# Kernel tuning notes

Hardware: AMD Instinct MI355X
Metric: run time of the kernel (lower is better)

The kernel has to match this reference:

```python
import jax, jax.numpy as jnp
import numpy as np

M_BUCKETS = 2048  # input_features // q = 4096 // 2


def countsketch(x, hash_idx, rand_sgn, m=M_BUCKETS):
    # x: [N, D]; scatter-add signed columns into m buckets -> [N, m]
    return jnp.zeros((x.shape[0], m), x.dtype).at[:, hash_idx].add(x * rand_sgn[None, :])


def setup_inputs() -> dict:
    key = jax.random.key(0)
    k1, k2, k3, k4, k5 = jax.random.split(key, 5)
    B, D, O = 4096, 4096, 4096
    inp = jax.random.normal(k1, (B, D), dtype=jnp.float32)
    # match torch init: weight uniform(-sqrt(3)/sqrt(D), sqrt(3)/sqrt(D)), bias uniform(-1/sqrt(D), 1/sqrt(D))
    bound = 1.0 / np.sqrt(D)
    weight = jax.random.uniform(k2, (O, D), dtype=jnp.float32,
                                minval=-bound * np.sqrt(3.0), maxval=bound * np.sqrt(3.0))
    bias = jax.random.uniform(k3, (O,), dtype=jnp.float32, minval=-bound, maxval=bound)
    hash_idx = jax.random.randint(k4, (D,), 0, M_BUCKETS, dtype=jnp.int32)
    rand_sgn = (2.0 * jax.random.randint(k5, (D,), 0, 2).astype(jnp.float32) - 1.0)
    return {"input": inp, "weight": weight, "bias": bias,
            "hash_idx": hash_idx, "rand_sgn": rand_sgn}


def reference(input, weight, bias, hash_idx, rand_sgn):
    input_sketch = countsketch(input, hash_idx, rand_sgn)    # [B, m]
    weight_sketch = countsketch(weight, hash_idx, rand_sgn)  # [O, m]
    out = input_sketch @ weight_sketch.T + bias[None, :]     # [B, O]
    return out
```

## Files before the change

### kernel.cpp

```cpp
#include <hip/hip_runtime.h>
#include <hip/hip_bf16.h>
#include <stdint.h>

#define D_DIM     4096
#define MB        2048
#define NROWS     4096
#define K_DIM     MB

typedef __bf16 bf16x8 __attribute__((ext_vector_type(8)));
typedef float  floatx4 __attribute__((ext_vector_type(4)));

__device__ __forceinline__ void gld_lds16(const void* g, void* l) {
    __builtin_amdgcn_global_load_lds(
        (const __attribute__((address_space(1))) unsigned int*)g,
        (__attribute__((address_space(3))) unsigned int*)l,
        16, 0, 0);
}

__global__ __launch_bounds__(256) void build_csr(
    const int* __restrict__ hash_idx,
    int* __restrict__ csr_off,
    int* __restrict__ csr_col)
{
    __shared__ int cnt[MB];
    __shared__ int scan[MB];
    const int t = threadIdx.x;

    for (int k = t; k < MB; k += 256) cnt[k] = 0;
    __syncthreads();
    for (int j = t; j < D_DIM; j += 256) atomicAdd(&cnt[hash_idx[j]], 1);
    __syncthreads();
    for (int k = t; k < MB; k += 256) scan[k] = cnt[k];
    __syncthreads();
    for (int stride = 1; stride < MB; stride <<= 1) {
        int vals[8];
        #pragma unroll
        for (int i = 0; i < 8; ++i) {
            int k = t + 256 * i;
            vals[i] = (k >= stride) ? scan[k - stride] : 0;
        }
        __syncthreads();
        #pragma unroll
        for (int i = 0; i < 8; ++i) scan[t + 256 * i] += vals[i];
        __syncthreads();
    }
    for (int k = t; k < MB; k += 256) csr_off[k] = scan[k] - cnt[k];
    if (t == 0) csr_off[MB] = scan[MB - 1];
    for (int k = t; k < MB; k += 256) cnt[k] = scan[k] - cnt[k];
    __syncthreads();
    for (int j = t; j < D_DIM; j += 256) {
        int k = hash_idx[j];
        int pos = atomicAdd(&cnt[k], 1);
        csr_col[pos] = j;
    }
}

__global__ __launch_bounds__(256) void sketch_kernel(
    const float* __restrict__ input,
    const float* __restrict__ weight,
    const float* __restrict__ rand_sgn,
    const int* __restrict__ csr_off,
    const int* __restrict__ csr_col,
    __hip_bfloat16* __restrict__ sk_in,
    __hip_bfloat16* __restrict__ sk_w)
{
    __shared__ float row[D_DIM];
    const int b = blockIdx.x;
    const bool is_w = (b >= NROWS);
    const int r = is_w ? (b - NROWS) : b;
    const float* src = (is_w ? weight : input) + (size_t)r * D_DIM;
    __hip_bfloat16* dst = (is_w ? sk_w : sk_in) + (size_t)r * MB;
    const int t = threadIdx.x;

    const float4* src4 = (const float4*)src;
    const float4* sgn4 = (const float4*)rand_sgn;
    #pragma unroll
    for (int i = 0; i < 4; ++i) {
        int idx = t + 256 * i;
        float4 x = src4[idx], s = sgn4[idx];
        row[4 * idx + 0] = x.x * s.x;
        row[4 * idx + 1] = x.y * s.y;
        row[4 * idx + 2] = x.z * s.z;
        row[4 * idx + 3] = x.w * s.w;
    }
    __syncthreads();

    #pragma unroll
    for (int i = 0; i < 8; ++i) {
        int k = t + 256 * i;
        int o0 = csr_off[k], o1 = csr_off[k + 1];
        float sum = 0.f;
        for (int p = o0; p < o1; ++p) sum += row[csr_col[p]];
        dst[k] = __float2bfloat16(sum);
    }
}

__global__ __launch_bounds__(256) void gemm_bt_bias(
    const __hip_bfloat16* __restrict__ A,
    const __hip_bfloat16* __restrict__ B,
    const float* __restrict__ bias,
    float* __restrict__ C)
{
    __shared__ __align__(16) __hip_bfloat16 lA[128 * 32];
    __shared__ __align__(16) __hip_bfloat16 lB[128 * 32];

    const int t = threadIdx.x;
    const int lane = t & 63;
    const int wid  = t >> 6;
    const int warpM = wid & 1, warpN = wid >> 1;
    const int quad = lane >> 4;
    const int mrow = lane & 15;
    const int rowBase = blockIdx.y * 128;
    const int colBase = blockIdx.x * 128;

    const int sr = t >> 2;
    const int sc = (t & 3) << 3;
    const __hip_bfloat16* gA = A + (size_t)(rowBase + sr) * K_DIM + sc;
    const __hip_bfloat16* gB = B + (size_t)(colBase + sr) * K_DIM + sc;
    __hip_bfloat16* sA = &lA[t * 8];
    __hip_bfloat16* sB = &lB[t * 8];

    floatx4 acc[4][4];
    const floatx4 zero = {0.f, 0.f, 0.f, 0.f};
    #pragma unroll
    for (int i = 0; i < 4; ++i)
        #pragma unroll
        for (int j = 0; j < 4; ++j) acc[i][j] = zero;

    for (int kb = 0; kb < K_DIM; kb += 32) {
        gld_lds16(gA + kb,                         sA);
        gld_lds16(gA + (size_t)64 * K_DIM + kb,    sA + 2048);
        gld_lds16(gB + kb,                         sB);
        gld_lds16(gB + (size_t)64 * K_DIM + kb,    sB + 2048);
        __syncthreads();

        bf16x8 af[4], bfr[4];
        #pragma unroll
        for (int i = 0; i < 4; ++i) {
            af[i]  = *(const bf16x8*)&lA[(warpM * 64 + i * 16 + mrow) * 32 + quad * 8];
            bfr[i] = *(const bf16x8*)&lB[(warpN * 64 + i * 16 + mrow) * 32 + quad * 8];
        }
        #pragma unroll
        for (int i = 0; i < 4; ++i)
            #pragma unroll
            for (int j = 0; j < 4; ++j)
                acc[i][j] = __builtin_amdgcn_mfma_f32_16x16x32_bf16(
                    af[i], bfr[j], acc[i][j], 0, 0, 0);
        __syncthreads();
    }

    float bj[4];
    #pragma unroll
    for (int j = 0; j < 4; ++j) bj[j] = bias[colBase + warpN * 64 + j * 16 + mrow];
    #pragma unroll
    for (int i = 0; i < 4; ++i) {
        int m0 = rowBase + warpM * 64 + i * 16 + quad * 4;
        #pragma unroll
        for (int j = 0; j < 4; ++j) {
            int n = colBase + warpN * 64 + j * 16 + mrow;
            #pragma unroll
            for (int p = 0; p < 4; ++p)
                C[(size_t)(m0 + p) * NROWS + n] = acc[i][j][p] + bj[j];
        }
    }
}

extern "C" void kernel_launch(void* const* d_in, const int* in_sizes, int n_in,
                              void* d_out, int out_size, void* d_ws, size_t ws_size,
                              hipStream_t stream) {
    const float* input  = (const float*)d_in[0];
    const float* weight = (const float*)d_in[1];
    const float* bias   = (const float*)d_in[2];
    const int*   hidx   = (const int*)d_in[3];
    const float* sgn    = (const float*)d_in[4];
    float* out = (float*)d_out;

    char* ws = (char*)d_ws;
    __hip_bfloat16* sk_in = (__hip_bfloat16*)ws;
    __hip_bfloat16* sk_w  = (__hip_bfloat16*)(ws + (size_t)16 * 1024 * 1024);
    int* csr_off = (int*)(ws + (size_t)32 * 1024 * 1024);
    int* csr_col = csr_off + 2064;

    build_csr<<<1, 256, 0, stream>>>(hidx, csr_off, csr_col);
    sketch_kernel<<<2 * NROWS, 256, 0, stream>>>(input, weight, sgn,
                                                 csr_off, csr_col, sk_in, sk_w);
    gemm_bt_bias<<<dim3(32, 32), 256, 0, stream>>>(sk_in, sk_w, bias, out);
}
```

Measured before the change: 311.2 us.

## Pack CSR descriptors, process two rows per sketch block, widen GEMM K-tile with swizzle

The bucket CSR is packed into one 32-bit descriptor (offset<<5 | count) plus 16-bit column indices, which are staged into LDS. Each sketch block now handles two rows, sharing the index lookups across both. The GEMM K-tile doubles to 64 and uses an XOR-swizzled LDS layout to avoid bank conflicts, halving the number of barriers per K. Risks are more LDS per sketch block, which lowers occupancy, and a 5-bit bucket count that overflows if any bucket holds more than 31 columns.

```diff
diff --git a/kernel.cpp b/kernel.cpp
--- a/kernel.cpp
+++ b/kernel.cpp
@@ -19,8 +19,8 @@
 
 __global__ __launch_bounds__(256) void build_csr(
     const int* __restrict__ hash_idx,
-    int* __restrict__ csr_off,
-    int* __restrict__ csr_col)
+    unsigned int* __restrict__ desc,
+    unsigned short* __restrict__ cols16)
 {
     __shared__ int cnt[MB];
     __shared__ int scan[MB];
@@ -44,54 +44,66 @@
         for (int i = 0; i < 8; ++i) scan[t + 256 * i] += vals[i];
         __syncthreads();
     }
-    for (int k = t; k < MB; k += 256) csr_off[k] = scan[k] - cnt[k];
-    if (t == 0) csr_off[MB] = scan[MB - 1];
-    for (int k = t; k < MB; k += 256) cnt[k] = scan[k] - cnt[k];
+    for (int k = t; k < MB; k += 256) {
+        int excl = scan[k] - cnt[k];
+        desc[k] = ((unsigned)excl << 5) | (unsigned)cnt[k];
+        cnt[k] = excl;
+    }
     __syncthreads();
     for (int j = t; j < D_DIM; j += 256) {
         int k = hash_idx[j];
         int pos = atomicAdd(&cnt[k], 1);
-        csr_col[pos] = j;
-    }
-}
-
-__global__ __launch_bounds__(256) void sketch_kernel(
+        cols16[pos] = (unsigned short)j;
+    }
+}
+
+__global__ __launch_bounds__(256) void sketch2(
     const float* __restrict__ input,
     const float* __restrict__ weight,
     const float* __restrict__ rand_sgn,
-    const int* __restrict__ csr_off,
-    const int* __restrict__ csr_col,
+    const unsigned int* __restrict__ desc,
+    const unsigned short* __restrict__ cols16,
     __hip_bfloat16* __restrict__ sk_in,
     __hip_bfloat16* __restrict__ sk_w)
 {
-    __shared__ float row[D_DIM];
+    __shared__ float rowAB[2 * D_DIM];
+    __shared__ __align__(16) unsigned short cols[D_DIM];
     const int b = blockIdx.x;
-    const bool is_w = (b >= NROWS);
-    const int r = is_w ? (b - NROWS) : b;
-    const float* src = (is_w ? weight : input) + (size_t)r * D_DIM;
-    __hip_bfloat16* dst = (is_w ? sk_w : sk_in) + (size_t)r * MB;
+    const bool is_w = (b >= NROWS / 2);
+    const int pr = is_w ? (b - NROWS / 2) : b;
+    const float* src = (is_w ? weight : input) + (size_t)pr * 2 * D_DIM;
+    __hip_bfloat16* dst = (is_w ? sk_w : sk_in) + (size_t)pr * 2 * MB;
     const int t = threadIdx.x;
 
-    const float4* src4 = (const float4*)src;
-    const float4* sgn4 = (const float4*)rand_sgn;
-    #pragma unroll
-    for (int i = 0; i < 4; ++i) {
-        int idx = t + 256 * i;
-        float4 x = src4[idx], s = sgn4[idx];
-        row[4 * idx + 0] = x.x * s.x;
-        row[4 * idx + 1] = x.y * s.y;
-        row[4 * idx + 2] = x.z * s.z;
-        row[4 * idx + 3] = x.w * s.w;
+    gld_lds16(cols16 + t * 8,         &cols[t * 8]);
+    gld_lds16(cols16 + (t + 256) * 8, &cols[(t + 256) * 8]);
+
+    const float4* s4 = (const float4*)src;
+    const float4* g4 = (const float4*)rand_sgn;
+    float4* r4 = (float4*)rowAB;
+    #pragma unroll
+    for (int p = 0; p < 8; ++p) {
+        int idx = t + 256 * p;
+        float4 x = s4[idx];
+        float4 g = g4[idx & 1023];
+        float4 y; y.x = x.x * g.x; y.y = x.y * g.y; y.z = x.z * g.z; y.w = x.w * g.w;
+        r4[idx] = y;
     }
     __syncthreads();
 
     #pragma unroll
     for (int i = 0; i < 8; ++i) {
         int k = t + 256 * i;
-        int o0 = csr_off[k], o1 = csr_off[k + 1];
-        float sum = 0.f;
-        for (int p = o0; p < o1; ++p) sum += row[csr_col[p]];
-        dst[k] = __float2bfloat16(sum);
+        unsigned d = desc[k];
+        int st = (int)(d >> 5), c = (int)(d & 31);
+        float s0 = 0.f, s1 = 0.f;
+        for (int p = 0; p < c; ++p) {
+            int j = cols[st + p];
+            s0 += rowAB[j];
+            s1 += rowAB[D_DIM + j];
+        }
+        dst[k]      = __float2bfloat16(s0);
+        dst[MB + k] = __float2bfloat16(s1);
     }
 }
 
@@ -101,8 +113,8 @@
     const float* __restrict__ bias,
     float* __restrict__ C)
 {
-    __shared__ __align__(16) __hip_bfloat16 lA[128 * 32];
-    __shared__ __align__(16) __hip_bfloat16 lB[128 * 32];
+    __shared__ __align__(16) __hip_bfloat16 lA[128 * 64];
+    __shared__ __align__(16) __hip_bfloat16 lB[128 * 64];
 
     const int t = threadIdx.x;
     const int lane = t & 63;
@@ -113,10 +125,16 @@
     const int rowBase = blockIdx.y * 128;
     const int colBase = blockIdx.x * 128;
 
-    const int sr = t >> 2;
-    const int sc = (t & 3) << 3;
-    const __hip_bfloat16* gA = A + (size_t)(rowBase + sr) * K_DIM + sc;
-    const __hip_bfloat16* gB = B + (size_t)(colBase + sr) * K_DIM + sc;
+    const __hip_bfloat16* gA[4];
+    const __hip_bfloat16* gB[4];
+    #pragma unroll
+    for (int p = 0; p < 4; ++p) {
+        int G = t + 256 * p;
+        int m = G >> 3;
+        int q = (G & 7) ^ (m & 7);
+        gA[p] = A + (size_t)(rowBase + m) * K_DIM + q * 8;
+        gB[p] = B + (size_t)(colBase + m) * K_DIM + q * 8;
+    }
     __hip_bfloat16* sA = &lA[t * 8];
     __hip_bfloat16* sB = &lB[t * 8];
 
@@ -127,25 +145,33 @@
         #pragma unroll
         for (int j = 0; j < 4; ++j) acc[i][j] = zero;
 
-    for (int kb = 0; kb < K_DIM; kb += 32) {
-        gld_lds16(gA + kb,                         sA);
-        gld_lds16(gA + (size_t)64 * K_DIM + kb,    sA + 2048);
-        gld_lds16(gB + kb,                         sB);
-        gld_lds16(gB + (size_t)64 * K_DIM + kb,    sB + 2048);
-        __syncthreads();
-
-        bf16x8 af[4], bfr[4];
-        #pragma unroll
-        for (int i = 0; i < 4; ++i) {
-            af[i]  = *(const bf16x8*)&lA[(warpM * 64 + i * 16 + mrow) * 32 + quad * 8];
-            bfr[i] = *(const bf16x8*)&lB[(warpN * 64 + i * 16 + mrow) * 32 + quad * 8];
-        }
-        #pragma unroll
-        for (int i = 0; i < 4; ++i)
+    for (int kb = 0; kb < K_DIM; kb += 64) {
+        #pragma unroll
+        for (int p = 0; p < 4; ++p) {
+            gld_lds16(gA[p] + kb, sA + p * 2048);
+            gld_lds16(gB[p] + kb, sB + p * 2048);
+        }
+        __syncthreads();
+
+        #pragma unroll
+        for (int h = 0; h < 2; ++h) {
+            bf16x8 af[4], bfr[4];
             #pragma unroll
-            for (int j = 0; j < 4; ++j)
-                acc[i][j] = __builtin_amdgcn_mfma_f32_16x16x32_bf16(
-                    af[i], bfr[j], acc[i][j], 0, 0, 0);
+            for (int i = 0; i < 4; ++i) {
+                int mA = warpM * 64 + i * 16 + mrow;
+                int sa = (h * 4 + quad) ^ (mA & 7);
+                af[i] = *(const bf16x8*)&lA[(mA * 8 + sa) * 8];
+                int mB = warpN * 64 + i * 16 + mrow;
+                int sb = (h * 4 + quad) ^ (mB & 7);
+                bfr[i] = *(const bf16x8*)&lB[(mB * 8 + sb) * 8];
+            }
+            #pragma unroll
+            for (int i = 0; i < 4; ++i)
+                #pragma unroll
+                for (int j = 0; j < 4; ++j)
+                    acc[i][j] = __builtin_amdgcn_mfma_f32_16x16x32_bf16(
+                        af[i], bfr[j], acc[i][j], 0, 0, 0);
+        }
         __syncthreads();
     }
 
@@ -178,11 +204,11 @@
     char* ws = (char*)d_ws;
     __hip_bfloat16* sk_in = (__hip_bfloat16*)ws;
     __hip_bfloat16* sk_w  = (__hip_bfloat16*)(ws + (size_t)16 * 1024 * 1024);
-    int* csr_off = (int*)(ws + (size_t)32 * 1024 * 1024);
-    int* csr_col = csr_off + 2064;
-
-    build_csr<<<1, 256, 0, stream>>>(hidx, csr_off, csr_col);
-    sketch_kernel<<<2 * NROWS, 256, 0, stream>>>(input, weight, sgn,
-                                                 csr_off, csr_col, sk_in, sk_w);
+    unsigned int*   desc  = (unsigned int*)(ws + (size_t)32 * 1024 * 1024);
+    unsigned short* cols16 = (unsigned short*)(ws + (size_t)32 * 1024 * 1024 + 8192);
+
+    build_csr<<<1, 256, 0, stream>>>(hidx, desc, cols16);
+    sketch2<<<NROWS, 256, 0, stream>>>(input, weight, sgn, desc, cols16,
+                                       sk_in, sk_w);
     gemm_bt_bias<<<dim3(32, 32), 256, 0, stream>>>(sk_in, sk_w, bias, out);
 }
```

After: 268.6 us. 1.16x faster.
